# Performance work log

Hardware: AMD Instinct MI355X
Metric: run time of the kernel (lower is better)

The kernel has to match this reference:

```python
import jax, jax.numpy as jnp
import numpy as np
from jax import lax

EPS = 1e-5
GROUPS = 16

def _conv(x, w, b):
    # x: [N,C,H,W], w: [O,I,3,3]
    y = lax.conv_general_dilated(x, w, (1, 1), 'SAME',
                                 dimension_numbers=('NCHW', 'OIHW', 'NCHW'))
    return y + b[None, :, None, None]

def _group_norm(x, gamma, beta):
    N, C, H, W = x.shape
    xr = x.reshape(N, GROUPS, C // GROUPS, H, W)
    m = xr.mean(axis=(2, 3, 4), keepdims=True)
    v = xr.var(axis=(2, 3, 4), keepdims=True)
    xn = ((xr - m) * lax.rsqrt(v + EPS)).reshape(N, C, H, W)
    return xn * gamma[None, :, None, None] + beta[None, :, None, None]

def _tower(x, ws, bs, gs, betas):
    for w, b, g, bt in zip(ws, bs, gs, betas):
        x = jax.nn.relu(_group_norm(_conv(x, w, b), g, bt))
    return x

def _fcos_heads(feats, cls_w, cls_b, cls_g, cls_bt, cls_ow, cls_ob,
                reg_w, reg_b, reg_g, reg_bt, reg_ow, reg_ob, ctr_w, ctr_b):
    outs = []
    for f in feats:
        N = f.shape[0]
        c = _tower(f, cls_w, cls_b, cls_g, cls_bt)
        logits = _conv(c, cls_ow, cls_ob)                 # [N, num_classes, H, W]
        r = _tower(f, reg_w, reg_b, reg_g, reg_bt)
        bbox = jax.nn.relu(_conv(r, reg_ow, reg_ob))      # [N, 4, H, W]
        ctr = _conv(r, ctr_w, ctr_b)                      # [N, 1, H, W]
        lvl = jnp.concatenate([logits, bbox, ctr], axis=1)  # [N, num_classes+5, H, W]
        outs.append(lvl.reshape(N, lvl.shape[1], -1))
    return jnp.concatenate(outs, axis=-1)  # [N, num_classes+5, sum(H*W)]

def setup_inputs() -> dict:
    key = jax.random.key(0)
    C, NUM_CLASSES, NB = 256, 80, 2
    sizes = [(128, 128), (64, 64), (32, 32), (16, 16), (8, 8)]
    keys = iter(jax.random.split(key, 64))
    d = {}
    for i, (h, w) in enumerate(sizes):
        d[f'feat{i}'] = jax.random.normal(next(keys), (NB, C, h, w), jnp.float32)
    for head in ('cls', 'reg'):
        for i in range(3):
            d[f'{head}_w{i}'] = 0.01 * jax.random.normal(next(keys), (C, C, 3, 3), jnp.float32)
            d[f'{head}_b{i}'] = jnp.zeros((C,), jnp.float32)
            d[f'{head}_gn_g{i}'] = jnp.ones((C,), jnp.float32)
            d[f'{head}_gn_b{i}'] = jnp.zeros((C,), jnp.float32)
    d['cls_out_w'] = 0.01 * jax.random.normal(next(keys), (NUM_CLASSES, C, 3, 3), jnp.float32)
    prior = 0.01
    d['cls_out_b'] = jnp.full((NUM_CLASSES,), float(-np.log((1 - prior) / prior)), jnp.float32)
    d['reg_out_w'] = 0.01 * jax.random.normal(next(keys), (4, C, 3, 3), jnp.float32)
    d['reg_out_b'] = jnp.zeros((4,), jnp.float32)
    d['ctr_w'] = 0.01 * jax.random.normal(next(keys), (1, C, 3, 3), jnp.float32)
    d['ctr_b'] = jnp.zeros((1,), jnp.float32)
    return d

def reference(feat0, feat1, feat2, feat3, feat4,
              cls_w0, cls_b0, cls_gn_g0, cls_gn_b0,
              cls_w1, cls_b1, cls_gn_g1, cls_gn_b1,
              cls_w2, cls_b2, cls_gn_g2, cls_gn_b2,
              reg_w0, reg_b0, reg_gn_g0, reg_gn_b0,
              reg_w1, reg_b1, reg_gn_g1, reg_gn_b1,
              reg_w2, reg_b2, reg_gn_g2, reg_gn_b2,
              cls_out_w, cls_out_b, reg_out_w, reg_out_b, ctr_w, ctr_b):
    feats = [feat0, feat1, feat2, feat3, feat4]
    return _fcos_heads(feats,
                       [cls_w0, cls_w1, cls_w2], [cls_b0, cls_b1, cls_b2],
                       [cls_gn_g0, cls_gn_g1, cls_gn_g2], [cls_gn_b0, cls_gn_b1, cls_gn_b2],
                       cls_out_w, cls_out_b,
                       [reg_w0, reg_w1, reg_w2], [reg_b0, reg_b1, reg_b2],
                       [reg_gn_g0, reg_gn_g1, reg_gn_g2], [reg_gn_b0, reg_gn_b1, reg_gn_b2],
                       reg_out_w, reg_out_b, ctr_w, ctr_b)
```

## Files before the change

kernel.cpp:

```cpp
#include <hip/hip_runtime.h>
#include <stdint.h>


typedef __attribute__((ext_vector_type(8))) short short8;
typedef __attribute__((ext_vector_type(4))) float floatx4;

#define XP 349184
#define TIB (32 * XP)

__device__ __forceinline__ unsigned short f2bf(float f) {
  unsigned u = __float_as_uint(f);
  u = (u + 0x7FFFu + ((u >> 16) & 1u)) >> 16;
  return (unsigned short)u;
}
__device__ __forceinline__ unsigned pk2(float a, float b) {
  return (unsigned)f2bf(a) | ((unsigned)f2bf(b) << 16);
}
__device__ __forceinline__ void async16(const void* g, void* l) {
  __builtin_amdgcn_global_load_lds(
      (const __attribute__((address_space(1))) unsigned int*)g,
      (__attribute__((address_space(3))) unsigned int*)l, 16, 0, 0);
}

#define WAIT_VM4 0x0F74
#define WAIT_VM0 0x0F70

__device__ const int d_lw[5]   = {7, 6, 5, 4, 3};
__device__ const int d_off[5]  = {0, 16384, 20480, 21504, 21760};
__device__ const int d_nt[5]   = {128, 32, 8, 2, 1};
__device__ const int d_cumT[6] = {0, 1024, 1280, 1344, 1360, 1368};
__device__ const int d_cumO[6] = {0, 512, 640, 672, 680, 684};
__device__ const int d_cumS[6] = {0, 256, 320, 336, 340, 341};

__global__ void zpk(float* zp, float* stats) {
  for (int i = threadIdx.x; i < 384; i += 256) zp[i] = 0.f;
  for (int i = threadIdx.x; i < 1920; i += 256) stats[i] = 0.f;
}

__global__ __launch_bounds__(256) void wtrans(
    const float* __restrict__ c0, const float* __restrict__ c1, const float* __restrict__ c2,
    const float* __restrict__ r0, const float* __restrict__ r1, const float* __restrict__ r2,
    const float* __restrict__ cw, const float* __restrict__ rw, const float* __restrict__ tw,
    unsigned short* __restrict__ dst) {
  const int z = blockIdx.y;
  const int nel = (z < 6) ? 589824 : 294912;
  const int idx = blockIdx.x * 256 + threadIdx.x;
  if (idx >= nel) return;
  int tmp = idx;
  const int j = tmp & 7;   tmp >>= 3;
  const int m = tmp & 127; tmp >>= 7;
  const int cs = tmp & 3;  tmp >>= 2;
  const int t = tmp % 9;   tmp /= 9;
  const int cc = tmp & 7;  const int mt = tmp >> 3;
  const int o = mt * 128 + m;
  const int i = cc * 32 + cs * 8 + j;
  float v = 0.f;
  const float* srcs[6] = {c0, c1, c2, r0, r1, r2};
  if (z < 6)      v = srcs[z][((size_t)o * 256 + i) * 9 + t];
  else if (z == 6){ if (o < 80) v = cw[((size_t)o * 256 + i) * 9 + t]; }
  else            { if (o < 4)  v = rw[((size_t)o * 256 + i) * 9 + t];
                    else if (o == 4) v = tw[(size_t)i * 9 + t]; }
  const size_t base = (z < 6) ? (size_t)z * 589824
                              : (size_t)6 * 589824 + (size_t)(z - 6) * 294912;
  dst[base + idx] = f2bf(v);
}

__global__ __launch_bounds__(256) void feat_nhwc(
    const float* __restrict__ s0, const float* __restrict__ s1,
    const float* __restrict__ s2, const float* __restrict__ s3,
    const float* __restrict__ s4, unsigned short* __restrict__ dst) {
  __shared__ unsigned short tile[64][65];
  int bx = blockIdx.x, lvl = 0;
  while (bx >= d_cumS[lvl + 1]) ++lvl;
  const int HW = 1 << (2 * d_lw[lvl]), off = d_off[lvl];
  const float* srcs[5] = {s0, s1, s2, s3, s4};
  const float* src = srcs[lvl];
  const int img = blockIdx.z, c0 = blockIdx.y * 64, p0 = (bx - d_cumS[lvl]) * 64;
  const float* s = src + ((size_t)img * 256 + c0) * HW + p0;
  const int tid = threadIdx.x;
#pragma unroll
  for (int i = 0; i < 4; i++) {
    const int cl = (tid >> 4) + i * 16, pl = (tid & 15) * 4;
    const float4 v = *(const float4*)(s + (size_t)cl * HW + pl);
    tile[cl][pl]     = f2bf(v.x);
    tile[cl][pl + 1] = f2bf(v.y);
    tile[cl][pl + 2] = f2bf(v.z);
    tile[cl][pl + 3] = f2bf(v.w);
  }
  __syncthreads();
  const int pl = tid >> 2, cseg = (tid & 3) * 16;
  unsigned ro[8];
#pragma unroll
  for (int k = 0; k < 8; k++)
    ro[k] = (unsigned)tile[cseg + 2 * k][pl] | ((unsigned)tile[cseg + 2 * k + 1][pl] << 16);
  const int ch0 = c0 + cseg;
  char* db = (char*)dst + (size_t)img * TIB + (size_t)(ch0 >> 3) * XP
           + (size_t)(off + p0 + pl) * 16;
  uint4 u0 = {ro[0], ro[1], ro[2], ro[3]};
  uint4 u1 = {ro[4], ro[5], ro[6], ro[7]};
  *(uint4*)db = u0;
  *(uint4*)(db + XP) = u1;
}

__global__ __launch_bounds__(256) void conv_mfma(
    const unsigned short* __restrict__ xin0, const unsigned short* __restrict__ xin1,
    const unsigned short* __restrict__ wA, const unsigned short* __restrict__ wB,
    unsigned short* __restrict__ y0, unsigned short* __restrict__ y1,
    const float* __restrict__ cb0, const float* __restrict__ cb1,
    float* __restrict__ out,
    const float* __restrict__ ob_cls, const float* __restrict__ ob_reg, const float* __restrict__ ob_ctr,
    const unsigned short* __restrict__ zp, int mode) {
  __shared__ __align__(16) char smem[49152];
  const int tid = threadIdx.x;
  const int* cum = (mode == 0) ? d_cumT : d_cumO;
  const int nwg = (mode == 0) ? 1368 : 684;
  const int xcd = blockIdx.x & 7, cidx = blockIdx.x >> 3;
  const int qq = nwg >> 3, rr = nwg & 7;
  int bid = (xcd < rr ? xcd * (qq + 1) : rr * (qq + 1) + (xcd - rr) * qq) + cidx;
  int lvl = 0;
  while (bid >= cum[lvl + 1]) ++lvl;
  int r = bid - cum[lvl];
  const int lw = d_lw[lvl], W = 1 << lw, HW = 1 << (2 * lw), poffl = d_off[lvl];
  const int ntc = d_nt[lvl];
  const int nt = r % ntc; r /= ntc;
  int mt = 0;
  if (mode == 0) { mt = r & 1; r >>= 1; }
  const int img = r & 1, tower = r >> 1;

  const unsigned short* xin = (tower ? xin1 : xin0) + (size_t)img * 21824 * 256;
  const unsigned short* wset = tower ? wB : wA;

  const int n = tid & 127;
  const int p = nt * 128 + n;
  const bool pv = p < HW;
  const int h = p >> lw, w = p & (W - 1);
  const int kq = tid >> 7;

  const char* xb = (const char*)xin;
  const char* tb[9];
  int stp[9];
#pragma unroll
  for (int t = 0; t < 9; t++) {
    const int rr2 = h + t / 3 - 1, cx = w + t % 3 - 1;
    const bool v = pv && rr2 >= 0 && rr2 < W && cx >= 0 && cx < W;
    tb[t] = v ? xb + (size_t)kq * XP + (size_t)(poffl + rr2 * W + cx) * 16
              : (const char*)zp;
    stp[t] = v ? 4 * XP : 0;
  }

  const char* abase = (const char*)wset + (size_t)mt * 589824;
  const char* a_tid = abase + (size_t)tid * 16;
  char* l_tid = smem + tid * 16;

  const int lane = tid & 63, q = lane >> 4, lr = lane & 15;
  const int wv = tid >> 6, wm = wv >> 1, wn = wv & 1;
  int aoff[4], boff[4];
#pragma unroll
  for (int i = 0; i < 4; i++) {
    aoff[i] = ((q << 7) + wm * 64 + i * 16 + lr) << 4;
    boff[i] = (((q << 7) + wn * 64 + i * 16 + lr) << 4) + 8192;
  }

  floatx4 acc[4][4];
#pragma unroll
  for (int i = 0; i < 4; i++)
#pragma unroll
    for (int j = 0; j < 4; j++) acc[i][j] = (floatx4){0.f, 0.f, 0.f, 0.f};

#define UNIT(CC, U, WIMM)                                                     \
  {                                                                           \
    const int it_ = (CC) * 9 + (U);                                           \
    __builtin_amdgcn_s_waitcnt(WIMM);                                         \
    __builtin_amdgcn_s_barrier();                                             \
    asm volatile("" ::: "memory");                                            \
    if (it_ + 2 < 72) {                                                       \
      const int nu_ = (U) + 2;                                                \
      const int tn_ = nu_ % 9;                              \
      const int ccn_ = (CC) + nu_ / 9;                                        \
      char* la_ = l_tid + (nu_ % 3) * 16384;                                  \
      const char* ap_ = a_tid + (size_t)(it_ + 2) * 8192;                     \
      async16(ap_, la_);                                                      \
      async16(ap_ + 4096, la_ + 4096);                                        \
      const int sp_ = stp[tn_];                                               \
      const char* bp_ = tb[tn_] + ccn_ * sp_;                                 \
      async16(bp_, la_ + 8192);                                               \
      async16(bp_ + (sp_ >> 1), la_ + 12288);                                 \
    }                                                                         \
    asm volatile("" ::: "memory");                                            \
    const int sb_ = ((U) % 3) * 16384;                                        \
    short8 af[4], bfr[4];                                                     \
    _Pragma("unroll")                                                         \
    for (int i = 0; i < 4; i++) {                                             \
      af[i] = *(const short8*)(smem + sb_ + aoff[i]);                         \
      bfr[i] = *(const short8*)(smem + sb_ + boff[i]);                        \
    }                                                                         \
    _Pragma("unroll")                                                         \
    for (int i = 0; i < 4; i++)                                               \
      _Pragma("unroll")                                                       \
      for (int j = 0; j < 4; j++)                                             \
        acc[i][j] = __builtin_amdgcn_mfma_f32_16x16x32_bf16(af[i], bfr[j],    \
                                                            acc[i][j], 0, 0, 0); \
  }

  async16(a_tid, l_tid);
  async16(a_tid + 4096, l_tid + 4096);
  async16(tb[0], l_tid + 8192);
  async16(tb[0] + (stp[0] >> 1), l_tid + 12288);
  async16(a_tid + 8192, l_tid + 16384);
  async16(a_tid + 12288, l_tid + 20480);
  async16(tb[1], l_tid + 24576);
  async16(tb[1] + (stp[1] >> 1), l_tid + 28672);

  for (int cc = 0; cc < 7; ++cc) {
#pragma unroll
    for (int u = 0; u < 9; ++u) UNIT(cc, u, WAIT_VM4)
  }
  UNIT(7, 0, WAIT_VM4) UNIT(7, 1, WAIT_VM4) UNIT(7, 2, WAIT_VM4)
  UNIT(7, 3, WAIT_VM4) UNIT(7, 4, WAIT_VM4) UNIT(7, 5, WAIT_VM4)
  UNIT(7, 6, WAIT_VM4) UNIT(7, 7, WAIT_VM0) UNIT(7, 8, WAIT_VM0)
#undef UNIT

  if (mode == 0) {
    unsigned short* y = (tower ? y1 : y0) + (size_t)img * 21824 * 256;
    const float* cb = tower ? cb1 : cb0;
#pragma unroll
    for (int j = 0; j < 4; j++) {
      const int pp = nt * 128 + wn * 64 + j * 16 + lr;
      if (pp >= HW) continue;
      unsigned short* yr = y + (size_t)(poffl + pp) * 256;
#pragma unroll
      for (int i = 0; i < 4; i++) {
        const int c = mt * 128 + wm * 64 + i * 16 + (q << 2);
        const float4 b4 = *(const float4*)(cb + c);
        floatx4 a = acc[i][j];
        uint2 u;
        u.x = pk2(a.x + b4.x, a.y + b4.y);
        u.y = pk2(a.z + b4.z, a.w + b4.w);
        *(uint2*)(yr + c) = u;
      }
    }
  } else {
#pragma unroll
    for (int j = 0; j < 4; j++) {
      const int pp = nt * 128 + wn * 64 + j * 16 + lr;
      if (pp >= HW) continue;
      const size_t gp = (size_t)poffl + pp;
#pragma unroll
      for (int i = 0; i < 4; i++) {
        const int m0 = wm * 64 + i * 16 + (q << 2);
        floatx4 a = acc[i][j];
#pragma unroll
        for (int k2 = 0; k2 < 4; k2++) {
          const int m = m0 + k2;
          const float v = a[k2];
          if (tower == 0) {
            if (m < 80) out[((size_t)img * 85 + m) * 21824 + gp] = v + ob_cls[m];
          } else {
            if (m < 4)
              out[((size_t)img * 85 + 80 + m) * 21824 + gp] = fmaxf(v + ob_reg[m], 0.f);
            else if (m == 4)
              out[((size_t)img * 85 + 84) * 21824 + gp] = v + ob_ctr[0];
          }
        }
      }
    }
  }
}

__global__ __launch_bounds__(256) void gn_stats(
    const unsigned short* __restrict__ y0, const unsigned short* __restrict__ y1,
    float* __restrict__ stats) {
  const int tz = blockIdx.z;
  const int tower = tz >> 1, img = tz & 1;
  int bx = blockIdx.x, lvl = 0;
  while (bx >= d_cumS[lvl + 1]) ++lvl;
  const int chunk = bx - d_cumS[lvl];
  const int off = d_off[lvl];
  const uint4* y = (const uint4*)((tower ? y1 : y0) + ((size_t)img * 21824 + off) * 256);
  const int tid = threadIdx.x;
  float s = 0.f, s2 = 0.f;
  const int e0 = chunk * 2048 + tid;
#pragma unroll
  for (int it = 0; it < 8; ++it) {
    const uint4 d = y[e0 + it * 256];
    unsigned uu[4] = {d.x, d.y, d.z, d.w};
#pragma unroll
    for (int k = 0; k < 4; k++) {
      const float f0 = __uint_as_float(uu[k] << 16);
      const float f1 = __uint_as_float(uu[k] & 0xFFFF0000u);
      s += f0 + f1;
      s2 += f0 * f0 + f1 * f1;
    }
  }
  s += __shfl_down(s, 32);
  s2 += __shfl_down(s2, 32);
  __shared__ float ls[4][32], lq[4][32];
  const int lane = tid & 63, wv = tid >> 6;
  if (lane < 32) { ls[wv][lane] = s; lq[wv][lane] = s2; }
  __syncthreads();
  if (tid < 32) {
    const float S = ls[0][tid] + ls[1][tid] + ls[2][tid] + ls[3][tid];
    const float Q = lq[0][tid] + lq[1][tid] + lq[2][tid] + lq[3][tid];
    ls[0][tid] = S; lq[0][tid] = Q;
  }
  __syncthreads();
  if (tid < 16) {
    float* st = stats + (((tz * 5 + lvl) * 16 + tid) << 1);
    atomicAdd(st, ls[0][2 * tid] + ls[0][2 * tid + 1]);
    atomicAdd(st + 1, lq[0][2 * tid] + lq[0][2 * tid + 1]);
  }
}

__global__ __launch_bounds__(256) void gn_apply(
    const unsigned short* __restrict__ ybase, unsigned short* __restrict__ xbase,
    const float* __restrict__ stats,
    const float* __restrict__ g0, const float* __restrict__ b0,
    const float* __restrict__ g1, const float* __restrict__ b1) {
  const int g = blockIdx.x * 256 + threadIdx.x;
  const int cc = ((g >> 1) & 3) * 2 + (g & 1);
  const int gg = g >> 3;
  const int pos = gg % 21824;
  const int ti = gg / 21824;
  const int tower = ti >> 1;
  const int lvl = (pos >= 16384) + (pos >= 20480) + (pos >= 21504) + (pos >= 21760);
  const float cnt = (float)(16 << (2 * d_lw[lvl]));
  const int cb = (ti * 5 + lvl) * 16 + cc * 2;
  float mean[2], rstd[2];
#pragma unroll
  for (int h2 = 0; h2 < 2; h2++) {
    const float m = stats[2 * (cb + h2)] / cnt;
    const float v = stats[2 * (cb + h2) + 1] / cnt - m * m;
    mean[h2] = m;
    rstd[h2] = rsqrtf(v + 1e-5f);
  }
  const float* gam = (tower ? g1 : g0) + cc * 32;
  const float* bet = (tower ? b1 : b0) + cc * 32;
  const uint4* yp = (const uint4*)(ybase + ((size_t)ti * 21824 + pos) * 256 + cc * 32);
  char* xb = (char*)xbase + (size_t)ti * TIB + (size_t)(cc * 4) * XP + (size_t)pos * 16;
#pragma unroll
  for (int q2 = 0; q2 < 4; q2++) {
    const uint4 d = yp[q2];
    const float m = mean[q2 >> 1], rs = rstd[q2 >> 1];
    unsigned uu[4] = {d.x, d.y, d.z, d.w};
    unsigned ro[4];
#pragma unroll
    for (int k = 0; k < 4; k++) {
      const float f0 = __uint_as_float(uu[k] << 16);
      const float f1 = __uint_as_float(uu[k] & 0xFFFF0000u);
      const float o0 = fmaxf((f0 - m) * rs * gam[q2 * 8 + 2 * k] + bet[q2 * 8 + 2 * k], 0.f);
      const float o1 = fmaxf((f1 - m) * rs * gam[q2 * 8 + 2 * k + 1] + bet[q2 * 8 + 2 * k + 1], 0.f);
      ro[k] = (unsigned)f2bf(o0) | ((unsigned)f2bf(o1) << 16);
    }
    uint4 od = {ro[0], ro[1], ro[2], ro[3]};
    *(uint4*)(xb + (size_t)q2 * XP) = od;
  }
}

extern "C" void kernel_launch(void* const* d_in, const int* in_sizes, int n_in,
                              void* d_out, int out_size, void* d_ws, size_t ws_size,
                              hipStream_t stream) {
  (void)in_sizes; (void)n_in; (void)out_size; (void)ws_size;
  char* ws = (char*)d_ws;
  unsigned short* zp = (unsigned short*)ws;
  unsigned short* wblk = (unsigned short*)(ws + 2048);
  const size_t WSET_T = 1179648;
  const size_t WSET_O = 589824;
  char* pXfeat = ws + 2048 + 6 * WSET_T + 2 * WSET_O;
  const size_t XSZ = (size_t)2 * 21824 * 256 * 2;
  char* pX = pXfeat + XSZ;
  char* pY = pX + 2 * XSZ;
  float* stats = (float*)(pY + 2 * XSZ);

  zpk<<<1, 256, 0, stream>>>((float*)zp, stats);
  wtrans<<<dim3(2304, 8), 256, 0, stream>>>(
      (const float*)d_in[5], (const float*)d_in[9], (const float*)d_in[13],
      (const float*)d_in[17], (const float*)d_in[21], (const float*)d_in[25],
      (const float*)d_in[29], (const float*)d_in[31], (const float*)d_in[33], wblk);
  feat_nhwc<<<dim3(341, 4, 2), 256, 0, stream>>>(
      (const float*)d_in[0], (const float*)d_in[1], (const float*)d_in[2],
      (const float*)d_in[3], (const float*)d_in[4], (unsigned short*)pXfeat);

  unsigned short* xc = (unsigned short*)pX;
  unsigned short* xr = (unsigned short*)(pX + XSZ);
  unsigned short* yc = (unsigned short*)pY;
  unsigned short* yr = (unsigned short*)(pY + XSZ);

  for (int s = 0; s < 3; s++) {
    const unsigned short* in0 = s ? xc : (unsigned short*)pXfeat;
    const unsigned short* in1 = s ? xr : (unsigned short*)pXfeat;
    const unsigned short* wc = wblk + (size_t)s * 589824;
    const unsigned short* wr = wblk + (size_t)(3 + s) * 589824;
    float* st_s = stats + (size_t)s * 640;
    conv_mfma<<<1368, 256, 0, stream>>>(
        in0, in1, wc, wr, yc, yr,
        (const float*)d_in[6 + 4 * s], (const float*)d_in[18 + 4 * s],
        nullptr, nullptr, nullptr, nullptr, zp, 0);
    gn_stats<<<dim3(341, 1, 4), 256, 0, stream>>>(yc, yr, st_s);
    gn_apply<<<2728, 256, 0, stream>>>(
        (const unsigned short*)pY, (unsigned short*)pX, st_s,
        (const float*)d_in[7 + 4 * s], (const float*)d_in[8 + 4 * s],
        (const float*)d_in[19 + 4 * s], (const float*)d_in[20 + 4 * s]);
  }
  const unsigned short* wo_c = wblk + (size_t)6 * 589824;
  const unsigned short* wo_r = wo_c + 294912;
  conv_mfma<<<684, 256, 0, stream>>>(
      xc, xr, wo_c, wo_r, nullptr, nullptr, nullptr, nullptr,
      (float*)d_out, (const float*)d_in[30], (const float*)d_in[32],
      (const float*)d_in[34], zp, 1);
}
```

Measured before the change: 637.3 us.

## Store conv output in channel-planar layout so GN passes read contiguous planes

The conv epilogue now writes pre-norm activations in the same 8-channel planar layout (plane stride XP) used for conv inputs, instead of pixel-major with 256 channels per row. gn_stats is regridded to per-group chunks over two planes, and gn_apply becomes a one-uint4-per-thread elementwise pass with identical input and output offsets. The aim is coalesced, uniform-stride access in the GN kernels and no transpose during apply, at the cost of scattered 8-byte stores in the conv epilogue and more, smaller GN blocks.

Measured after the change: 600.6 us. -5.8%, faster.

```diff
diff --git a/kernel.cpp b/kernel.cpp
--- a/kernel.cpp
+++ b/kernel.cpp
@@ -31,6 +31,9 @@
 __device__ const int d_cumT[6] = {0, 1024, 1280, 1344, 1360, 1368};
 __device__ const int d_cumO[6] = {0, 512, 640, 672, 680, 684};
 __device__ const int d_cumS[6] = {0, 256, 320, 336, 340, 341};
+__device__ const int ck_lvl[13] = {0,0,0,0,0,0,0,0,1,1,2,3,4};
+__device__ const int ck_c0[13]  = {0,2048,4096,6144,8192,10240,12288,14336,0,2048,0,0,0};
+__device__ const int ck_len[13] = {2048,2048,2048,2048,2048,2048,2048,2048,2048,2048,1024,256,64};
 
 __global__ void zpk(float* zp, float* stats) {
   for (int i = threadIdx.x; i < 384; i += 256) zp[i] = 0.f;
@@ -221,22 +224,22 @@
 #undef UNIT
 
   if (mode == 0) {
-    unsigned short* y = (tower ? y1 : y0) + (size_t)img * 21824 * 256;
+    char* yb = (char*)(tower ? y1 : y0) + (size_t)img * TIB;
     const float* cb = tower ? cb1 : cb0;
 #pragma unroll
-    for (int j = 0; j < 4; j++) {
-      const int pp = nt * 128 + wn * 64 + j * 16 + lr;
-      if (pp >= HW) continue;
-      unsigned short* yr = y + (size_t)(poffl + pp) * 256;
-#pragma unroll
-      for (int i = 0; i < 4; i++) {
-        const int c = mt * 128 + wm * 64 + i * 16 + (q << 2);
-        const float4 b4 = *(const float4*)(cb + c);
+    for (int i = 0; i < 4; i++) {
+      const int c = mt * 128 + wm * 64 + i * 16 + (q << 2);
+      const float4 b4 = *(const float4*)(cb + c);
+      char* yp = yb + (size_t)(c >> 3) * XP + (size_t)poffl * 16 + ((c & 7) << 1);
+#pragma unroll
+      for (int j = 0; j < 4; j++) {
+        const int pp = nt * 128 + wn * 64 + j * 16 + lr;
+        if (pp >= HW) continue;
         floatx4 a = acc[i][j];
         uint2 u;
         u.x = pk2(a.x + b4.x, a.y + b4.y);
         u.y = pk2(a.z + b4.z, a.w + b4.w);
-        *(uint2*)(yr + c) = u;
+        *(uint2*)(yp + (size_t)pp * 16) = u;
       }
     }
   } else {
@@ -270,19 +273,18 @@
 __global__ __launch_bounds__(256) void gn_stats(
     const unsigned short* __restrict__ y0, const unsigned short* __restrict__ y1,
     float* __restrict__ stats) {
-  const int tz = blockIdx.z;
+  const int ck = blockIdx.x, g = blockIdx.y, tz = blockIdx.z;
   const int tower = tz >> 1, img = tz & 1;
-  int bx = blockIdx.x, lvl = 0;
-  while (bx >= d_cumS[lvl + 1]) ++lvl;
-  const int chunk = bx - d_cumS[lvl];
-  const int off = d_off[lvl];
-  const uint4* y = (const uint4*)((tower ? y1 : y0) + ((size_t)img * 21824 + off) * 256);
+  const int lvl = ck_lvl[ck], c0 = ck_c0[ck], len = ck_len[ck];
+  const char* base = (const char*)(tower ? y1 : y0) + (size_t)img * TIB
+                   + (size_t)(2 * g) * XP + (size_t)(d_off[lvl] + c0) * 16;
   const int tid = threadIdx.x;
   float s = 0.f, s2 = 0.f;
-  const int e0 = chunk * 2048 + tid;
-#pragma unroll
-  for (int it = 0; it < 8; ++it) {
-    const uint4 d = y[e0 + it * 256];
+  const int n2 = 2 * len;
+  for (int i = tid; i < n2; i += 256) {
+    const int pl = (i >= len);
+    const int pos = i - pl * len;
+    const uint4 d = *(const uint4*)(base + (size_t)pl * XP + (size_t)pos * 16);
     unsigned uu[4] = {d.x, d.y, d.z, d.w};
 #pragma unroll
     for (int k = 0; k < 4; k++) {
@@ -292,22 +294,19 @@
       s2 += f0 * f0 + f1 * f1;
     }
   }
-  s += __shfl_down(s, 32);
-  s2 += __shfl_down(s2, 32);
-  __shared__ float ls[4][32], lq[4][32];
-  const int lane = tid & 63, wv = tid >> 6;
-  if (lane < 32) { ls[wv][lane] = s; lq[wv][lane] = s2; }
+#pragma unroll
+  for (int m = 1; m < 64; m <<= 1) {
+    s += __shfl_xor(s, m);
+    s2 += __shfl_xor(s2, m);
+  }
+  __shared__ float rs[4], rq[4];
+  const int lane = tid & 63, wvv = tid >> 6;
+  if (lane == 0) { rs[wvv] = s; rq[wvv] = s2; }
   __syncthreads();
-  if (tid < 32) {
-    const float S = ls[0][tid] + ls[1][tid] + ls[2][tid] + ls[3][tid];
-    const float Q = lq[0][tid] + lq[1][tid] + lq[2][tid] + lq[3][tid];
-    ls[0][tid] = S; lq[0][tid] = Q;
-  }
-  __syncthreads();
-  if (tid < 16) {
-    float* st = stats + (((tz * 5 + lvl) * 16 + tid) << 1);
-    atomicAdd(st, ls[0][2 * tid] + ls[0][2 * tid + 1]);
-    atomicAdd(st + 1, lq[0][2 * tid] + lq[0][2 * tid + 1]);
+  if (tid == 0) {
+    float* st = stats + (((tz * 5 + lvl) * 16 + g) << 1);
+    atomicAdd(st, rs[0] + rs[1] + rs[2] + rs[3]);
+    atomicAdd(st + 1, rq[0] + rq[1] + rq[2] + rq[3]);
   }
 }
 
@@ -317,43 +316,33 @@
     const float* __restrict__ g0, const float* __restrict__ b0,
     const float* __restrict__ g1, const float* __restrict__ b1) {
   const int g = blockIdx.x * 256 + threadIdx.x;
-  const int cc = ((g >> 1) & 3) * 2 + (g & 1);
-  const int gg = g >> 3;
-  const int pos = gg % 21824;
-  const int ti = gg / 21824;
+  const int pos = g % 21824;
+  const int rest = g / 21824;
+  const int plane = rest & 31;
+  const int ti = rest >> 5;
   const int tower = ti >> 1;
   const int lvl = (pos >= 16384) + (pos >= 20480) + (pos >= 21504) + (pos >= 21760);
   const float cnt = (float)(16 << (2 * d_lw[lvl]));
-  const int cb = (ti * 5 + lvl) * 16 + cc * 2;
-  float mean[2], rstd[2];
-#pragma unroll
-  for (int h2 = 0; h2 < 2; h2++) {
-    const float m = stats[2 * (cb + h2)] / cnt;
-    const float v = stats[2 * (cb + h2) + 1] / cnt - m * m;
-    mean[h2] = m;
-    rstd[h2] = rsqrtf(v + 1e-5f);
-  }
-  const float* gam = (tower ? g1 : g0) + cc * 32;
-  const float* bet = (tower ? b1 : b0) + cc * 32;
-  const uint4* yp = (const uint4*)(ybase + ((size_t)ti * 21824 + pos) * 256 + cc * 32);
-  char* xb = (char*)xbase + (size_t)ti * TIB + (size_t)(cc * 4) * XP + (size_t)pos * 16;
-#pragma unroll
-  for (int q2 = 0; q2 < 4; q2++) {
-    const uint4 d = yp[q2];
-    const float m = mean[q2 >> 1], rs = rstd[q2 >> 1];
-    unsigned uu[4] = {d.x, d.y, d.z, d.w};
-    unsigned ro[4];
-#pragma unroll
-    for (int k = 0; k < 4; k++) {
-      const float f0 = __uint_as_float(uu[k] << 16);
-      const float f1 = __uint_as_float(uu[k] & 0xFFFF0000u);
-      const float o0 = fmaxf((f0 - m) * rs * gam[q2 * 8 + 2 * k] + bet[q2 * 8 + 2 * k], 0.f);
-      const float o1 = fmaxf((f1 - m) * rs * gam[q2 * 8 + 2 * k + 1] + bet[q2 * 8 + 2 * k + 1], 0.f);
-      ro[k] = (unsigned)f2bf(o0) | ((unsigned)f2bf(o1) << 16);
-    }
-    uint4 od = {ro[0], ro[1], ro[2], ro[3]};
-    *(uint4*)(xb + (size_t)q2 * XP) = od;
-  }
+  const float* st = stats + ((((ti * 5 + lvl) * 16 + (plane >> 1))) << 1);
+  const float mean = st[0] / cnt;
+  const float var = st[1] / cnt - mean * mean;
+  const float rstd = rsqrtf(var + 1e-5f);
+  const float* gam = (tower ? g1 : g0) + plane * 8;
+  const float* bet = (tower ? b1 : b0) + plane * 8;
+  const size_t off = (size_t)ti * TIB + (size_t)plane * XP + (size_t)pos * 16;
+  const uint4 d = *(const uint4*)((const char*)ybase + off);
+  unsigned uu[4] = {d.x, d.y, d.z, d.w};
+  unsigned ro[4];
+#pragma unroll
+  for (int k = 0; k < 4; k++) {
+    const float f0 = __uint_as_float(uu[k] << 16);
+    const float f1 = __uint_as_float(uu[k] & 0xFFFF0000u);
+    const float o0 = fmaxf((f0 - mean) * rstd * gam[2 * k] + bet[2 * k], 0.f);
+    const float o1 = fmaxf((f1 - mean) * rstd * gam[2 * k + 1] + bet[2 * k + 1], 0.f);
+    ro[k] = (unsigned)f2bf(o0) | ((unsigned)f2bf(o1) << 16);
+  }
+  uint4 od = {ro[0], ro[1], ro[2], ro[3]};
+  *(uint4*)((char*)xbase + off) = od;
 }
 
 extern "C" void kernel_launch(void* const* d_in, const int* in_sizes, int n_in,
@@ -395,8 +384,8 @@
         in0, in1, wc, wr, yc, yr,
         (const float*)d_in[6 + 4 * s], (const float*)d_in[18 + 4 * s],
         nullptr, nullptr, nullptr, nullptr, zp, 0);
-    gn_stats<<<dim3(341, 1, 4), 256, 0, stream>>>(yc, yr, st_s);
-    gn_apply<<<2728, 256, 0, stream>>>(
+    gn_stats<<<dim3(13, 16, 4), 256, 0, stream>>>(yc, yr, st_s);
+    gn_apply<<<10912, 256, 0, stream>>>(
         (const unsigned short*)pY, (unsigned short*)pX, st_s,
         (const float*)d_in[7 + 4 * s], (const float*)d_in[8 + 4 * s],
         (const float*)d_in[19 + 4 * s], (const float*)d_in[20 + 4 * s]);
```
